# Optimization experiments

Hardware: AMD Instinct MI355X
Metric: run time of the kernel (lower is better)

The kernel has to match this reference:

```python
import jax, jax.numpy as jnp
import numpy as np

DIM = 1024
NUM_HEAVY = 1024
N_ITERS = 50
EPS = 1.0
FETCH_K_RATIO = 9.0 / 8.0


def rms_norm(x, gamma):
    # F.normalize(x, dim=-1) * sqrt(d) * gamma
    norm = jnp.maximum(jnp.linalg.norm(x, axis=-1, keepdims=True), 1e-12)
    return (x / norm) * (x.shape[-1] ** 0.5) * gamma


def feed_forward(x, gamma, w1, b1, w2, b2):
    h = jax.nn.gelu(rms_norm(x, gamma) @ w1 + b1, approximate=False)
    return h @ w2 + b2


def coor_descent(s, k, n_iters, eps):
    # Wright et al. coordinate descent routing scores (eps_decay=1 -> constant eps)
    logk = jnp.log(jnp.asarray(k, dtype=s.dtype))

    def step(ab, _):
        a, b = ab
        sb = (s + b) / eps
        a = eps * (logk - jax.scipy.special.logsumexp(sb, axis=-1, keepdims=True))
        b = -jax.nn.relu(s + a)
        return (a, b), None

    a0 = jnp.zeros_like(s[..., :1])
    b0 = -s
    (a, b), _ = jax.lax.scan(step, (a0, b0), None, length=n_iters)
    return jnp.exp((s + a + b) / eps)


def setup_inputs() -> dict:
    key = jax.random.key(0)
    ks = jax.random.split(key, 8)
    b, n, d = 4, 8192, DIM
    dl, dh = int(d * 0.5), d * 4
    u = lambda k, shape, fan_in: jax.random.uniform(k, shape, jnp.float32, -1.0, 1.0) / np.sqrt(fan_in)
    return {
        "x": jax.random.normal(ks[0], (b, n, d), jnp.float32),
        "routing_token": jax.random.normal(ks[1], (d,), jnp.float32),
        "light_gamma": jnp.ones((d,), jnp.float32),
        "light_w1": u(ks[2], (d, dl), d),
        "light_b1": jnp.zeros((dl,), jnp.float32),
        "light_w2": u(ks[3], (dl, d), dl),
        "light_b2": jnp.zeros((d,), jnp.float32),
        "heavy_gamma": jnp.ones((d,), jnp.float32),
        "heavy_w1": u(ks[4], (d, dh), d),
        "heavy_b1": jnp.zeros((dh,), jnp.float32),
        "heavy_w2": u(ks[5], (dh, d), dh),
        "heavy_b2": jnp.zeros((d,), jnp.float32),
    }


def reference(x, routing_token, light_gamma, light_w1, light_b1, light_w2, light_b2,
              heavy_gamma, heavy_w1, heavy_b1, heavy_w2, heavy_b2):
    b, n, d = x.shape
    # light branch over all tokens
    light_out = feed_forward(x, light_gamma, light_w1, light_b1, light_w2, light_b2)

    # coordinate-descent router (single routing token)
    s = jnp.einsum('bnd,d->bn', x, routing_token)
    effective_k = min(NUM_HEAVY * FETCH_K_RATIO, n)
    scores = coor_descent(s, effective_k, N_ITERS, EPS)
    sel_scores, sel_idx = jax.lax.top_k(scores, NUM_HEAVY)  # [b, k]
    # straight-through: forward value 1.0, gradient flows through sel_scores
    sel_scores = sel_scores + jax.lax.stop_gradient(1.0 - sel_scores)

    # gather -> heavy FFN -> scale -> scatter back
    routed = jnp.take_along_axis(x, sel_idx[..., None], axis=1)  # [b, k, d]
    routed_out = feed_forward(routed, heavy_gamma, heavy_w1, heavy_b1, heavy_w2, heavy_b2)
    routed_out = routed_out * sel_scores[..., None]
    batch_idx = jnp.arange(b)[:, None]
    heavy_out = jnp.zeros_like(x).at[batch_idx, sel_idx].set(routed_out)

    return light_out + heavy_out
```

## Files before the change

kernel.cpp:

```cpp
#include <hip/hip_runtime.h>
#include <hip/hip_bf16.h>
#include <math.h>

#define DIMD   1024
#define NBATCH 4
#define NSEQ   8192
#define NTOK   (NBATCH * NSEQ)
#define NHEAVY 1024
#define NSEL   (NBATCH * NHEAVY)
#define DLIGHT 512
#define DHEAVY 4096
#define NITERS 50
#define BK     64

typedef __attribute__((ext_vector_type(8))) short short8;
typedef __attribute__((ext_vector_type(4))) float f32x4;
typedef __attribute__((ext_vector_type(4))) unsigned short u16x4;

__device__ __forceinline__ unsigned short f2bf(float f) {
    __hip_bfloat16 h = __float2bfloat16(f);
    union { __hip_bfloat16 h; unsigned short u; } cvt;
    cvt.h = h;
    return cvt.u;
}

__device__ __forceinline__ float bf2f(unsigned short u) {
    return __uint_as_float((unsigned)u << 16);
}

__device__ __forceinline__ float gelu_fast(float x) {
    float ax = fabsf(x) * 0.7071067811865475f;
    float t = 1.0f / fmaf(0.3275911f, ax, 1.0f);
    float p = fmaf(t, 1.061405429f, -1.453152027f);
    p = fmaf(t, p, 1.421413741f);
    p = fmaf(t, p, -0.284496736f);
    p = fmaf(t, p, 0.254829592f);
    p = p * t;
    float e = __expf(-ax * ax);
    float erf_abs = fmaf(-p, e, 1.0f);
    float erf = copysignf(erf_abs, x);
    return 0.5f * x * (1.0f + erf);
}

__device__ __forceinline__ void gload_lds16(const void* g, void* l) {
    __builtin_amdgcn_global_load_lds(
        (const __attribute__((address_space(1))) void*)g,
        (__attribute__((address_space(3))) void*)l,
        16, 0, 0);
}

__global__ __launch_bounds__(256) void fused_init(
    const float* __restrict__ lw1, const float* __restrict__ lw2,
    const float* __restrict__ hw1, const float* __restrict__ hw2,
    const float* __restrict__ lgamma, const float* __restrict__ hgamma,
    short* __restrict__ wl1t, short* __restrict__ wl2t,
    short* __restrict__ wh1t, short* __restrict__ wh2t,
    const float* __restrict__ x, const float* __restrict__ rt,
    unsigned short* __restrict__ xb, float* __restrict__ sc,
    double* __restrict__ s_out) {
    __shared__ float tile[32][33];
    __shared__ float red[4];
    __shared__ double redd[4];
    int b = blockIdx.x;
    int tid = threadIdx.x;

    const float* cin = nullptr; short* cout = nullptr; const float* cg = nullptr;
    int cK = 0, cN = 0, cnx = 0, cb = 0;
    if (b < 512)        { cin = lw1; cout = wl1t; cg = lgamma; cK = DIMD;   cN = DLIGHT; cnx = 16;  cb = b; }
    else if (b < 1024)  { cin = lw2; cout = wl2t; cg = nullptr; cK = DLIGHT; cN = DIMD;  cnx = 32;  cb = b - 512; }
    else if (b < 5120)  { cin = hw1; cout = wh1t; cg = hgamma; cK = DIMD;   cN = DHEAVY; cnx = 128; cb = b - 1024; }
    else if (b < 9216)  { cin = hw2; cout = wh2t; cg = nullptr; cK = DHEAVY; cN = DIMD;  cnx = 32;  cb = b - 5120; }

    if (cin) {
        int n0 = (cb % cnx) * 32, k0 = (cb / cnx) * 32;
        int tx = tid & 31, ty = tid >> 5;
        #pragma unroll
        for (int j = 0; j < 4; j++) {
            int k = k0 + ty + 8 * j;
            float g = cg ? cg[k] : 1.0f;
            tile[ty + 8 * j][tx] = cin[(size_t)k * cN + (n0 + tx)] * g;
        }
        __syncthreads();
        #pragma unroll
        for (int j = 0; j < 4; j++)
            cout[(size_t)(n0 + ty + 8 * j) * cK + (k0 + tx)] =
                (short)f2bf(tile[tx][ty + 8 * j]);
        return;
    }

    int t = b - 9216;
    const float4* xr = (const float4*)(x + (size_t)t * DIMD);
    float4 v = xr[tid];
    ushort4 pk;
    pk.x = f2bf(v.x); pk.y = f2bf(v.y); pk.z = f2bf(v.z); pk.w = f2bf(v.w);
    ((ushort4*)(xb + (size_t)t * DIMD))[tid] = pk;

    float ss = v.x * v.x + v.y * v.y + v.z * v.z + v.w * v.w;
    float4 rv = ((const float4*)rt)[tid];
    double sd = (double)v.x * rv.x + (double)v.y * rv.y + (double)v.z * rv.z + (double)v.w * rv.w;
    #pragma unroll
    for (int off = 32; off > 0; off >>= 1) {
        ss += __shfl_down(ss, off);
        sd += __shfl_down(sd, off);
    }
    if ((tid & 63) == 0) { red[tid >> 6] = ss; redd[tid >> 6] = sd; }
    __syncthreads();
    if (tid == 0) {
        s_out[t] = redd[0] + redd[1] + redd[2] + redd[3];
        float tot = red[0] + red[1] + red[2] + red[3];
        sc[t] = 32.0f / fmaxf(sqrtf(tot), 1e-12f);
    }
}

__global__ __launch_bounds__(256) void mega_kern(
    const double* __restrict__ s, double* __restrict__ a_out,
    const short* __restrict__ A, const short* __restrict__ Bt,
    const float* __restrict__ bias, const float* __restrict__ sc,
    __hip_bfloat16* __restrict__ outb) {
    __shared__ alignas(16) short As[2][128 * 64];
    __shared__ alignas(16) short Bs[2][128 * 64];
    __shared__ double redd[2][4];
    int tid = threadIdx.x;

    if (blockIdx.x < 4) {
        int r = blockIdx.x;
        int l = tid & 63, w = tid >> 6;
        const double* sr = s + (size_t)r * NSEQ;
        double es[32];
        #pragma unroll
        for (int i = 0; i < 32; i++) es[i] = exp(sr[tid + i * 256]);
        const double Kk = 1152.0;
        double ea = exp(log(Kk) - log((double)NSEQ));
        for (int it = 1; it < NITERS; it++) {
            double loc = 0.0;
            #pragma unroll
            for (int i = 0; i < 32; i++) {
                double p = es[i] * ea;
                loc += (p < 1.0 ? p : 1.0);
            }
            #pragma unroll
            for (int off = 32; off > 0; off >>= 1) loc += __shfl_down(loc, off);
            int pb = it & 1;
            if (l == 0) redd[pb][w] = loc;
            __syncthreads();
            double S = redd[pb][0] + redd[pb][1] + redd[pb][2] + redd[pb][3];
            ea = ea * (Kk / S);
        }
        if (tid == 0) a_out[r] = log(ea);
        return;
    }

    const int N = DLIGHT, K = DIMD;
    int gid = blockIdx.x - 4;
    int id = (gid & 7) * (1024 >> 3) + (gid >> 3);
    int nx = N / 128;
    int bxi = id % nx, byi = id / nx;
    int l = tid & 63, w = tid >> 6;
    int wr = w >> 1, wc = w & 1;
    int bn0 = bxi * 128, bm0 = byi * 128;

    f32x4 zero = {0.f, 0.f, 0.f, 0.f};
    f32x4 acc[4][4];
    #pragma unroll
    for (int i = 0; i < 4; i++)
        #pragma unroll
        for (int j = 0; j < 4; j++) acc[i][j] = zero;

    const int lrow = l & 15, lk = (l >> 4) * 8;
    int srow = tid >> 3, scol = (tid & 7) * 8;
    const short* AgC[4];
    const short* BgC[4];
    #pragma unroll
    for (int c = 0; c < 4; c++) {
        AgC[c] = A + (size_t)(bm0 + srow + c * 32) * K + scol;
        BgC[c] = Bt + (size_t)(bn0 + srow + c * 32) * K + scol;
    }
    const int sbase = (tid & ~63) * 8;

    auto stage = [&](int b, int k0) {
        #pragma unroll
        for (int c = 0; c < 4; c++) {
            gload_lds16(AgC[c] + k0, &As[b][sbase + c * 2048]);
            gload_lds16(BgC[c] + k0, &Bs[b][sbase + c * 2048]);
        }
    };

    int nt = K / 64;
    stage(0, 0);
    for (int t = 0; t < nt; ++t) {
        int cur = t & 1;
        if (t + 1 < nt) {
            stage(cur ^ 1, (t + 1) * 64);
            asm volatile("s_waitcnt vmcnt(8)" ::: "memory");
        } else {
            asm volatile("s_waitcnt vmcnt(0)" ::: "memory");
        }
        __builtin_amdgcn_s_barrier();
        asm volatile("" ::: "memory");
        #pragma unroll
        for (int kk = 0; kk < 2; kk++) {
            short8 af[4], bf[4];
            #pragma unroll
            for (int i = 0; i < 4; i++) {
                af[i] = *reinterpret_cast<const short8*>(&As[cur][(wr * 64 + i * 16 + lrow) * 64 + kk * 32 + lk]);
                bf[i] = *reinterpret_cast<const short8*>(&Bs[cur][(wc * 64 + i * 16 + lrow) * 64 + kk * 32 + lk]);
            }
            #pragma unroll
            for (int mi = 0; mi < 4; mi++)
                #pragma unroll
                for (int ni = 0; ni < 4; ni++)
                    acc[mi][ni] = __builtin_amdgcn_mfma_f32_16x16x32_bf16(bf[ni], af[mi], acc[mi][ni], 0, 0, 0);
        }
        if (t + 1 < nt) {
            asm volatile("" ::: "memory");
            __builtin_amdgcn_s_barrier();
            asm volatile("" ::: "memory");
        }
    }

    int orow0 = bm0 + wr * 64, ocol0 = bn0 + wc * 64;
    const int lr = l & 15, lq = (l >> 4) * 4;
    #pragma unroll
    for (int mi = 0; mi < 4; mi++) {
        int row = orow0 + mi * 16 + lr;
        float scv = sc[row];
        #pragma unroll
        for (int ni = 0; ni < 4; ni++) {
            int c0 = ocol0 + ni * 16 + lq;
            f32x4 bv = *reinterpret_cast<const f32x4*>(bias + c0);
            u16x4 pk;
            #pragma unroll
            for (int rg = 0; rg < 4; rg++)
                pk[rg] = f2bf(gelu_fast(fmaf(scv, acc[mi][ni][rg], bv[rg])));
            *reinterpret_cast<u16x4*>((unsigned short*)outb + (size_t)row * N + c0) = pk;
        }
    }
}

__global__ void select_kern(const double* __restrict__ s, const double* __restrict__ a_arr,
                            int* __restrict__ sel, int* __restrict__ inv) {
    int r = blockIdx.x, l = threadIdx.x;
    const double* sr = s + (size_t)r * NSEQ;
    double a = a_arr[r];
    __shared__ double sw[NSEQ];
    int cnt = 0;
    for (int base = 0; base < NSEQ; base += 64) {
        int idx = base + l;
        double v = sr[idx];
        bool sat = (v + a) >= 0.0;
        sw[idx] = sat ? -1.0e300 : v;
        unsigned long long m = __ballot(sat);
        int pre = __popcll(m & ((1ull << l) - 1ull));
        if (sat) {
            int slot = cnt + pre;
            if (slot < NHEAVY) {
                sel[r * NHEAVY + slot] = r * NSEQ + idx;
                inv[r * NSEQ + idx] = r * NHEAVY + slot;
            }
        }
        cnt += (int)__popcll(m);
    }
    __syncthreads();
    for (int slot = cnt; slot < NHEAVY; slot++) {
        double best = -1.0e301; int bidx = NSEQ;
        for (int i = 0; i < NSEQ / 64; i++) {
            int idx = i * 64 + l;
            double v = sw[idx];
            if (v > best) { best = v; bidx = idx; }
        }
        #pragma unroll
        for (int off = 32; off > 0; off >>= 1) {
            double ov = __shfl_down(best, off);
            int oi = __shfl_down(bidx, off);
            if (ov > best || (ov == best && oi < bidx)) { best = ov; bidx = oi; }
        }
        bidx = __shfl(bidx, 0);
        if (l == 0) {
            sel[r * NHEAVY + slot] = r * NSEQ + bidx;
            inv[r * NSEQ + bidx] = r * NHEAVY + slot;
            sw[bidx] = -1.0e300;
        }
        __syncthreads();
    }
}

__global__ __launch_bounds__(256) void reduce_hv_kern(
    const unsigned short* __restrict__ phb, const float* __restrict__ hb2,
    float* __restrict__ hv, int nsk) {
    int h = blockIdx.x;
    int c0 = threadIdx.x * 4;
    f32x4 acc = *reinterpret_cast<const f32x4*>(hb2 + c0);
    for (int j = 0; j < nsk; j++) {
        u16x4 p = *reinterpret_cast<const u16x4*>(phb + ((size_t)j * NSEL + h) * DIMD + c0);
        #pragma unroll
        for (int rg = 0; rg < 4; rg++) acc[rg] += bf2f(p[rg]);
    }
    *reinterpret_cast<f32x4*>(hv + (size_t)h * DIMD + c0) = acc;
}

template <int EPI, bool GATHER>
__global__ __launch_bounds__(512) void gemm256(
    const short* __restrict__ A, const short* __restrict__ Bt,
    const float* __restrict__ bias,
    const float* __restrict__ sc, const int* __restrict__ sel,
    const int* __restrict__ inv, const float* __restrict__ hv,
    float* __restrict__ outf, __hip_bfloat16* __restrict__ outb,
    int M, int N, int K) {
    __shared__ alignas(16) short As[2][2][128 * 64];
    __shared__ alignas(16) short Bs[2][2][128 * 64];

    int nx = gridDim.x, ny = gridDim.y;
    int nwg = nx * ny * gridDim.z;
    int id = ((int)blockIdx.z * ny + blockIdx.y) * nx + blockIdx.x;
    if ((nwg & 7) == 0) id = (id & 7) * (nwg >> 3) + (id >> 3);
    int bxi = id % nx; int rem = id / nx;
    int byi = rem % ny; int bz = rem / ny;
    int klen = K / (int)gridDim.z, k0base = bz * klen;
    int bn0 = bxi * 256, bm0 = byi * 256;

    int tid = threadIdx.x;
    int l = tid & 63, w = tid >> 6;
    int wr = w >> 2, wc = w & 3;

    f32x4 zero = {0.f, 0.f, 0.f, 0.f};
    f32x4 acc[8][4];
    #pragma unroll
    for (int i = 0; i < 8; i++)
        #pragma unroll
        for (int j = 0; j < 4; j++) acc[i][j] = zero;

    const short* aSrc[2][2];
    const short* bSrc[2][2];
    #pragma unroll
    for (int h = 0; h < 2; h++)
        #pragma unroll
        for (int j = 0; j < 2; j++) {
            int p = j * 8192 + tid * 16;
            int o = p ^ (((p >> 7) & 7) << 4);
            int lrow = o >> 7, colb = o & 127;
            int agrow = bm0 + h * 128 + lrow;
            int garow = GATHER ? sel[agrow] : agrow;
            aSrc[h][j] = A + (size_t)garow * K + (colb >> 1);
            bSrc[h][j] = Bt + (size_t)(bn0 + h * 128 + lrow) * K + (colb >> 1);
        }

    auto stageA = [&](int b, int h, int kof) {
        #pragma unroll
        for (int j = 0; j < 2; j++)
            gload_lds16(aSrc[h][j] + kof, &As[b][h][j * 4096 + w * 512]);
    };
    auto stageB = [&](int b, int h, int kof) {
        #pragma unroll
        for (int j = 0; j < 2; j++)
            gload_lds16(bSrc[h][j] + kof, &Bs[b][h][j * 4096 + w * 512]);
    };

    int nt = klen / BK;
    stageA(0, 0, k0base); stageA(0, 1, k0base);
    stageB(0, 0, k0base); stageB(0, 1, k0base);
    if (nt > 1) {
        stageB(1, 0, k0base + BK); stageB(1, 1, k0base + BK);
        asm volatile("s_waitcnt vmcnt(4)" ::: "memory");
    } else {
        asm volatile("s_waitcnt vmcnt(0)" ::: "memory");
    }
    __builtin_amdgcn_s_barrier();

    const int lr = l & 15;
    const int swz = (lr & 7) << 4;
    const int rbase = lr * 128;
    const int colk[2] = { (((l >> 4) * 16)) ^ swz, (((l >> 4) * 16) + 64) ^ swz };

    short8 bfr[4][2];
    for (int t = 0; t < nt; ++t) {
        int d = t & 1;
        const char* aHalf = (const char*)(&As[d][wr][0]);
        const char* bHalf = (const char*)(&Bs[d][wc >> 1][0]) + (wc & 1) * 8192;
        #pragma unroll
        for (int q = 0; q < 4; q++) {
            if (q == 0) {
                #pragma unroll
                for (int ni = 0; ni < 4; ni++)
                    #pragma unroll
                    for (int kk = 0; kk < 2; kk++)
                        bfr[ni][kk] = *reinterpret_cast<const short8*>(bHalf + rbase + ni * 2048 + colk[kk]);
            }
            short8 afr[2][2];
            #pragma unroll
            for (int m2 = 0; m2 < 2; m2++)
                #pragma unroll
                for (int kk = 0; kk < 2; kk++)
                    afr[m2][kk] = *reinterpret_cast<const short8*>(aHalf + rbase + (q * 2 + m2) * 2048 + colk[kk]);
            if (q == 0 && t + 1 < nt) stageA(d ^ 1, 0, k0base + (t + 1) * BK);
            else if (q == 1 && t + 1 < nt) stageA(d ^ 1, 1, k0base + (t + 1) * BK);
            else if (q == 2 && t + 2 < nt) stageB(d, 0, k0base + (t + 2) * BK);
            else if (q == 3 && t + 2 < nt) stageB(d, 1, k0base + (t + 2) * BK);
            if (q == 3) {
                if (t + 2 < nt) asm volatile("s_waitcnt vmcnt(4)" ::: "memory");
                else            asm volatile("s_waitcnt vmcnt(0)" ::: "memory");
            }
            __builtin_amdgcn_s_barrier();
            asm volatile("s_waitcnt lgkmcnt(0)" ::: "memory");
            __builtin_amdgcn_sched_barrier(0);
            __builtin_amdgcn_s_setprio(1);
            #pragma unroll
            for (int m2 = 0; m2 < 2; m2++)
                #pragma unroll
                for (int ni = 0; ni < 4; ni++)
                    #pragma unroll
                    for (int kk = 0; kk < 2; kk++)
                        acc[q * 2 + m2][ni] = __builtin_amdgcn_mfma_f32_16x16x32_bf16(
                            bfr[ni][kk], afr[m2][kk], acc[q * 2 + m2][ni], 0, 0, 0);
            __builtin_amdgcn_s_setprio(0);
            __builtin_amdgcn_s_barrier();
        }
    }

    int orow0 = bm0 + wr * 128, ocol0 = bn0 + wc * 64;
    const int lq = (l >> 4) * 4;
    #pragma unroll
    for (int mi = 0; mi < 8; mi++) {
        int row = orow0 + mi * 16 + lr;
        float scv = 0.0f;
        int iv = -1;
        if (EPI == 0) scv = sc[GATHER ? sel[row] : row];
        if (EPI == 3) iv = inv[row];
        #pragma unroll
        for (int ni = 0; ni < 4; ni++) {
            int c0 = ocol0 + ni * 16 + lq;
            if (EPI == 0) {
                f32x4 bv = *reinterpret_cast<const f32x4*>(bias + c0);
                u16x4 pk;
                #pragma unroll
                for (int rg = 0; rg < 4; rg++)
                    pk[rg] = f2bf(gelu_fast(fmaf(scv, acc[mi][ni][rg], bv[rg])));
                *reinterpret_cast<u16x4*>((unsigned short*)outb + (size_t)row * N + c0) = pk;
            } else if (EPI == 2) {
                u16x4 pk;
                #pragma unroll
                for (int rg = 0; rg < 4; rg++) pk[rg] = f2bf(acc[mi][ni][rg]);
                *reinterpret_cast<u16x4*>((unsigned short*)outb + ((size_t)bz * M + row) * (size_t)N + c0) = pk;
            } else {
                f32x4 bv = *reinterpret_cast<const f32x4*>(bias + c0);
                f32x4 v = acc[mi][ni] + bv;
                if (iv >= 0) {
                    f32x4 hvv = *reinterpret_cast<const f32x4*>(hv + (size_t)iv * DIMD + c0);
                    v = v + hvv;
                }
                __builtin_nontemporal_store(v, reinterpret_cast<f32x4*>(outf + (size_t)row * N + c0));
            }
        }
    }
}

extern "C" void kernel_launch(void* const* d_in, const int* in_sizes, int n_in,
                              void* d_out, int out_size, void* d_ws, size_t ws_size,
                              hipStream_t stream) {
    (void)in_sizes; (void)n_in; (void)out_size;
    const float* x      = (const float*)d_in[0];
    const float* rt     = (const float*)d_in[1];
    const float* lgamma = (const float*)d_in[2];
    const float* lw1    = (const float*)d_in[3];
    const float* lb1    = (const float*)d_in[4];
    const float* lw2    = (const float*)d_in[5];
    const float* lb2    = (const float*)d_in[6];
    const float* hgamma = (const float*)d_in[7];
    const float* hw1    = (const float*)d_in[8];
    const float* hb1    = (const float*)d_in[9];
    const float* hw2    = (const float*)d_in[10];
    const float* hb2    = (const float*)d_in[11];
    float* out = (float*)d_out;

    auto rnd = [](size_t b) { return (b + 255) & ~(size_t)255; };
    size_t fixed = rnd(NTOK * sizeof(double))
                 + rnd(256)
                 + rnd(NSEL * sizeof(int))
                 + rnd(NTOK * sizeof(int))
                 + rnd(NTOK * sizeof(float))
                 + rnd((size_t)DLIGHT * DIMD * 2)
                 + rnd((size_t)DIMD * DLIGHT * 2)
                 + rnd((size_t)DHEAVY * DIMD * 2)
                 + rnd((size_t)DIMD * DHEAVY * 2)
                 + rnd((size_t)NTOK * DIMD * 2)
                 + rnd((size_t)NSEL * DHEAVY * 2)
                 + rnd((size_t)NTOK * DLIGHT * 2)
                 + rnd((size_t)NSEL * DIMD * 4);
    int nsk = 4;
    while (nsk > 1 && fixed + rnd((size_t)nsk * NSEL * DIMD * 2) > ws_size) nsk >>= 1;

    char* base = (char*)d_ws;
    size_t off = 0;
    auto alloc = [&](size_t bytes) -> void* {
        void* p = base + off;
        off += rnd(bytes);
        return p;
    };
    double* s     = (double*)alloc(NTOK * sizeof(double));
    double* a_arr = (double*)alloc(256);
    int*    sel   = (int*)alloc(NSEL * sizeof(int));
    int*    inv   = (int*)alloc(NTOK * sizeof(int));
    float*  sc    = (float*)alloc(NTOK * sizeof(float));
    short*  wl1t  = (short*)alloc((size_t)DLIGHT * DIMD * 2);
    short*  wl2t  = (short*)alloc((size_t)DIMD * DLIGHT * 2);
    short*  wh1t  = (short*)alloc((size_t)DHEAVY * DIMD * 2);
    short*  wh2t  = (short*)alloc((size_t)DIMD * DHEAVY * 2);
    short*  xb    = (short*)alloc((size_t)NTOK * DIMD * 2);
    short*  hh    = (short*)alloc((size_t)NSEL * DHEAVY * 2);
    short*  hl    = (short*)alloc((size_t)NTOK * DLIGHT * 2);
    float*  hv    = (float*)alloc((size_t)NSEL * DIMD * 4);
    short*  phb   = (short*)alloc((size_t)nsk * NSEL * DIMD * 2);

    hipMemsetAsync(inv, 0xFF, NTOK * sizeof(int), stream);

    fused_init<<<9216 + NTOK, 256, 0, stream>>>(
        lw1, lw2, hw1, hw2, lgamma, hgamma,
        wl1t, wl2t, wh1t, wh2t,
        x, rt, (unsigned short*)xb, sc, s);

    mega_kern<<<4 + 1024, 256, 0, stream>>>(
        s, a_arr, xb, wl1t, lb1, sc, (__hip_bfloat16*)hl);

    select_kern<<<NBATCH, 64, 0, stream>>>(s, a_arr, sel, inv);

    gemm256<0, true><<<dim3(DHEAVY / 256, NSEL / 256), 512, 0, stream>>>(
        xb, wh1t, hb1, sc, sel, nullptr, nullptr,
        nullptr, (__hip_bfloat16*)hh, NSEL, DHEAVY, DIMD);
    gemm256<2, false><<<dim3(DIMD / 256, NSEL / 256, nsk), 512, 0, stream>>>(
        hh, wh2t, nullptr, nullptr, nullptr, nullptr, nullptr,
        nullptr, (__hip_bfloat16*)phb, NSEL, DIMD, DHEAVY);
    reduce_hv_kern<<<NSEL, 256, 0, stream>>>((const unsigned short*)phb, hb2, hv, nsk);

    gemm256<3, false><<<dim3(DIMD / 256, NTOK / 256), 512, 0, stream>>>(
        hl, wl2t, lb2, nullptr, nullptr, inv, hv,
        out, nullptr, NTOK, DIMD, DLIGHT);
}
```

Measured before the change: 340.7 us.

## Fuse top-k selection into router blocks and restructure gemm256 inner phases

The separate select kernel is folded into the four coordinate-descent blocks of mega_kern, so selection runs concurrently with the light GEMM and one launch disappears. The memset of the inverse index is replaced by a per-token write in fused_init. The gemm256 main loop goes from four quarter phases to two half phases, issuing both A stages together and then both B stages, which halves the barriers per K-step but keeps more fragment registers live. The shared memory is rearranged into one raw buffer so the selection scratch can reuse the GEMM tiles.

```diff
diff --git a/kernel.cpp b/kernel.cpp
--- a/kernel.cpp
+++ b/kernel.cpp
@@ -57,7 +57,7 @@
     short* __restrict__ wh1t, short* __restrict__ wh2t,
     const float* __restrict__ x, const float* __restrict__ rt,
     unsigned short* __restrict__ xb, float* __restrict__ sc,
-    double* __restrict__ s_out) {
+    double* __restrict__ s_out, int* __restrict__ inv) {
     __shared__ float tile[32][33];
     __shared__ float red[4];
     __shared__ double redd[4];
@@ -109,22 +109,24 @@
         s_out[t] = redd[0] + redd[1] + redd[2] + redd[3];
         float tot = red[0] + red[1] + red[2] + red[3];
         sc[t] = 32.0f / fmaxf(sqrtf(tot), 1e-12f);
+        inv[t] = -1;
     }
 }
 
 __global__ __launch_bounds__(256) void mega_kern(
-    const double* __restrict__ s, double* __restrict__ a_out,
+    const double* __restrict__ s, int* __restrict__ sel, int* __restrict__ inv,
     const short* __restrict__ A, const short* __restrict__ Bt,
     const float* __restrict__ bias, const float* __restrict__ sc,
     __hip_bfloat16* __restrict__ outb) {
-    __shared__ alignas(16) short As[2][128 * 64];
-    __shared__ alignas(16) short Bs[2][128 * 64];
-    __shared__ double redd[2][4];
+    __shared__ alignas(16) char smem[65536 + 64];
+    short (*As)[128 * 64] = reinterpret_cast<short (*)[128 * 64]>(smem);
+    short (*Bs)[128 * 64] = reinterpret_cast<short (*)[128 * 64]>(smem + 32768);
     int tid = threadIdx.x;
 
     if (blockIdx.x < 4) {
         int r = blockIdx.x;
-        int l = tid & 63, w = tid >> 6;
+        int lw = tid & 63, w = tid >> 6;
+        double* redd = (double*)(smem + 65536);
         const double* sr = s + (size_t)r * NSEQ;
         double es[32];
         #pragma unroll
@@ -140,13 +142,55 @@
             }
             #pragma unroll
             for (int off = 32; off > 0; off >>= 1) loc += __shfl_down(loc, off);
-            int pb = it & 1;
-            if (l == 0) redd[pb][w] = loc;
+            int pb = (it & 1) * 4;
+            if (lw == 0) redd[pb + w] = loc;
             __syncthreads();
-            double S = redd[pb][0] + redd[pb][1] + redd[pb][2] + redd[pb][3];
+            double S = redd[pb] + redd[pb + 1] + redd[pb + 2] + redd[pb + 3];
             ea = ea * (Kk / S);
         }
-        if (tid == 0) a_out[r] = log(ea);
+        double a = log(ea);
+        __syncthreads();
+        if (tid >= 64) return;
+
+        int l = tid;
+        double* sw = (double*)smem;
+        int cnt = 0;
+        for (int base = 0; base < NSEQ; base += 64) {
+            int idx = base + l;
+            double v = sr[idx];
+            bool sat = (v + a) >= 0.0;
+            sw[idx] = sat ? -1.0e300 : v;
+            unsigned long long m = __ballot(sat);
+            int pre = __popcll(m & ((1ull << l) - 1ull));
+            if (sat) {
+                int slot = cnt + pre;
+                if (slot < NHEAVY) {
+                    sel[r * NHEAVY + slot] = r * NSEQ + idx;
+                    inv[r * NSEQ + idx] = r * NHEAVY + slot;
+                }
+            }
+            cnt += (int)__popcll(m);
+        }
+        for (int slot = cnt; slot < NHEAVY; slot++) {
+            double best = -1.0e301; int bidx = NSEQ;
+            for (int i = 0; i < NSEQ / 64; i++) {
+                int idx = i * 64 + l;
+                double v = sw[idx];
+                if (v > best) { best = v; bidx = idx; }
+            }
+            #pragma unroll
+            for (int off = 32; off > 0; off >>= 1) {
+                double ov = __shfl_down(best, off);
+                int oi = __shfl_down(bidx, off);
+                if (ov > best || (ov == best && oi < bidx)) { best = ov; bidx = oi; }
+            }
+            bidx = __shfl(bidx, 0);
+            if (l == 0) {
+                sel[r * NHEAVY + slot] = r * NSEQ + bidx;
+                inv[r * NSEQ + bidx] = r * NHEAVY + slot;
+                sw[bidx] = -1.0e300;
+            }
+        }
         return;
     }
 
@@ -234,53 +278,6 @@
                 pk[rg] = f2bf(gelu_fast(fmaf(scv, acc[mi][ni][rg], bv[rg])));
             *reinterpret_cast<u16x4*>((unsigned short*)outb + (size_t)row * N + c0) = pk;
         }
-    }
-}
-
-__global__ void select_kern(const double* __restrict__ s, const double* __restrict__ a_arr,
-                            int* __restrict__ sel, int* __restrict__ inv) {
-    int r = blockIdx.x, l = threadIdx.x;
-    const double* sr = s + (size_t)r * NSEQ;
-    double a = a_arr[r];
-    __shared__ double sw[NSEQ];
-    int cnt = 0;
-    for (int base = 0; base < NSEQ; base += 64) {
-        int idx = base + l;
-        double v = sr[idx];
-        bool sat = (v + a) >= 0.0;
-        sw[idx] = sat ? -1.0e300 : v;
-        unsigned long long m = __ballot(sat);
-        int pre = __popcll(m & ((1ull << l) - 1ull));
-        if (sat) {
-            int slot = cnt + pre;
-            if (slot < NHEAVY) {
-                sel[r * NHEAVY + slot] = r * NSEQ + idx;
-                inv[r * NSEQ + idx] = r * NHEAVY + slot;
-            }
-        }
-        cnt += (int)__popcll(m);
-    }
-    __syncthreads();
-    for (int slot = cnt; slot < NHEAVY; slot++) {
-        double best = -1.0e301; int bidx = NSEQ;
-        for (int i = 0; i < NSEQ / 64; i++) {
-            int idx = i * 64 + l;
-            double v = sw[idx];
-            if (v > best) { best = v; bidx = idx; }
-        }
-        #pragma unroll
-        for (int off = 32; off > 0; off >>= 1) {
-            double ov = __shfl_down(best, off);
-            int oi = __shfl_down(bidx, off);
-            if (ov > best || (ov == best && oi < bidx)) { best = ov; bidx = oi; }
-        }
-        bidx = __shfl(bidx, 0);
-        if (l == 0) {
-            sel[r * NHEAVY + slot] = r * NSEQ + bidx;
-            inv[r * NSEQ + bidx] = r * NHEAVY + slot;
-            sw[bidx] = -1.0e300;
-        }
-        __syncthreads();
     }
 }
 
@@ -377,40 +374,45 @@
         const char* aHalf = (const char*)(&As[d][wr][0]);
         const char* bHalf = (const char*)(&Bs[d][wc >> 1][0]) + (wc & 1) * 8192;
         #pragma unroll
-        for (int q = 0; q < 4; q++) {
-            if (q == 0) {
+        for (int ph = 0; ph < 2; ph++) {
+            if (ph == 0) {
                 #pragma unroll
                 for (int ni = 0; ni < 4; ni++)
                     #pragma unroll
                     for (int kk = 0; kk < 2; kk++)
                         bfr[ni][kk] = *reinterpret_cast<const short8*>(bHalf + rbase + ni * 2048 + colk[kk]);
             }
-            short8 afr[2][2];
-            #pragma unroll
-            for (int m2 = 0; m2 < 2; m2++)
+            short8 afr[4][2];
+            #pragma unroll
+            for (int m2 = 0; m2 < 4; m2++)
                 #pragma unroll
                 for (int kk = 0; kk < 2; kk++)
-                    afr[m2][kk] = *reinterpret_cast<const short8*>(aHalf + rbase + (q * 2 + m2) * 2048 + colk[kk]);
-            if (q == 0 && t + 1 < nt) stageA(d ^ 1, 0, k0base + (t + 1) * BK);
-            else if (q == 1 && t + 1 < nt) stageA(d ^ 1, 1, k0base + (t + 1) * BK);
-            else if (q == 2 && t + 2 < nt) stageB(d, 0, k0base + (t + 2) * BK);
-            else if (q == 3 && t + 2 < nt) stageB(d, 1, k0base + (t + 2) * BK);
-            if (q == 3) {
-                if (t + 2 < nt) asm volatile("s_waitcnt vmcnt(4)" ::: "memory");
-                else            asm volatile("s_waitcnt vmcnt(0)" ::: "memory");
+                    afr[m2][kk] = *reinterpret_cast<const short8*>(aHalf + rbase + (ph * 4 + m2) * 2048 + colk[kk]);
+            if (ph == 0) {
+                if (t + 1 < nt) {
+                    stageA(d ^ 1, 0, k0base + (t + 1) * BK);
+                    stageA(d ^ 1, 1, k0base + (t + 1) * BK);
+                }
+            } else {
+                if (t + 2 < nt) {
+                    stageB(d, 0, k0base + (t + 2) * BK);
+                    stageB(d, 1, k0base + (t + 2) * BK);
+                    asm volatile("s_waitcnt vmcnt(4)" ::: "memory");
+                } else {
+                    asm volatile("s_waitcnt vmcnt(0)" ::: "memory");
+                }
             }
             __builtin_amdgcn_s_barrier();
             asm volatile("s_waitcnt lgkmcnt(0)" ::: "memory");
-            __builtin_amdgcn_sched_barrier(0);
             __builtin_amdgcn_s_setprio(1);
             #pragma unroll
-            for (int m2 = 0; m2 < 2; m2++)
+            for (int m2 = 0; m2 < 4; m2++)
                 #pragma unroll
                 for (int ni = 0; ni < 4; ni++)
                     #pragma unroll
                     for (int kk = 0; kk < 2; kk++)
-                        acc[q * 2 + m2][ni] = __builtin_amdgcn_mfma_f32_16x16x32_bf16(
-                            bfr[ni][kk], afr[m2][kk], acc[q * 2 + m2][ni], 0, 0, 0);
+                        acc[ph * 4 + m2][ni] = __builtin_amdgcn_mfma_f32_16x16x32_bf16(
+                            bfr[ni][kk], afr[m2][kk], acc[ph * 4 + m2][ni], 0, 0, 0);
             __builtin_amdgcn_s_setprio(0);
             __builtin_amdgcn_s_barrier();
         }
@@ -473,7 +475,6 @@
 
     auto rnd = [](size_t b) { return (b + 255) & ~(size_t)255; };
     size_t fixed = rnd(NTOK * sizeof(double))
-                 + rnd(256)
                  + rnd(NSEL * sizeof(int))
                  + rnd(NTOK * sizeof(int))
                  + rnd(NTOK * sizeof(float))
@@ -496,7 +497,6 @@
         return p;
     };
     double* s     = (double*)alloc(NTOK * sizeof(double));
-    double* a_arr = (double*)alloc(256);
     int*    sel   = (int*)alloc(NSEL * sizeof(int));
     int*    inv   = (int*)alloc(NTOK * sizeof(int));
     float*  sc    = (float*)alloc(NTOK * sizeof(float));
@@ -510,17 +510,13 @@
     float*  hv    = (float*)alloc((size_t)NSEL * DIMD * 4);
     short*  phb   = (short*)alloc((size_t)nsk * NSEL * DIMD * 2);
 
-    hipMemsetAsync(inv, 0xFF, NTOK * sizeof(int), stream);
-
     fused_init<<<9216 + NTOK, 256, 0, stream>>>(
         lw1, lw2, hw1, hw2, lgamma, hgamma,
         wl1t, wl2t, wh1t, wh2t,
-        x, rt, (unsigned short*)xb, sc, s);
+        x, rt, (unsigned short*)xb, sc, s, inv);
 
     mega_kern<<<4 + 1024, 256, 0, stream>>>(
-        s, a_arr, xb, wl1t, lb1, sc, (__hip_bfloat16*)hl);
-
-    select_kern<<<NBATCH, 64, 0, stream>>>(s, a_arr, sel, inv);
+        s, sel, inv, xb, wl1t, lb1, sc, (__hip_bfloat16*)hl);
 
     gemm256<0, true><<<dim3(DHEAVY / 256, NSEL / 256), 512, 0, stream>>>(
         xb, wh1t, hb1, sc, sel, nullptr, nullptr,
```

Measured after the change: 291.8 us. -14.3%, faster.
